# Optimization experiments

Measured on AMD Instinct MI355X. Metric: run time of the kernel, lower is better.

## Reference

```python
import math
import jax, jax.numpy as jnp
import numpy as np
from jax import lax

# FPN anchor layout: 1024x768 image, strides {4,8,16,32,64}, 3 anchors/location
NUM_PER_LEVEL = (147456, 36864, 9216, 2304, 576)
A_TOTAL = sum(NUM_PER_LEVEL)
BATCH = 8
PRE_NMS_TOP_N = 1000   # testing
POST_NMS_TOP_N = 1000  # testing
NMS_THRESH = 0.7
SCORE_THRESH = 0.0
MIN_SIZE = 1.0
IMG_H, IMG_W = 768.0, 1024.0
BBOX_XFORM_CLIP = math.log(1000.0 / 16.0)


def setup_inputs() -> dict:
    key = jax.random.key(0)
    k1, k2, k3, k4, k5, k6 = jax.random.split(key, 6)
    objectness = jax.random.normal(k1, (BATCH, A_TOTAL), jnp.float32)
    pred_bbox_deltas = jax.random.normal(k2, (BATCH, A_TOTAL, 4), jnp.float32) * 0.2
    # valid anchor boxes (x1, y1, x2, y2)
    cx = jax.random.uniform(k3, (A_TOTAL,), jnp.float32) * IMG_W
    cy = jax.random.uniform(k4, (A_TOTAL,), jnp.float32) * IMG_H
    w = 16.0 + jax.random.uniform(k5, (A_TOTAL,), jnp.float32) * 176.0
    h = 16.0 + jax.random.uniform(k6, (A_TOTAL,), jnp.float32) * 176.0
    anchors = jnp.stack([cx - 0.5 * w, cy - 0.5 * h, cx + 0.5 * w, cy + 0.5 * h], -1)
    return {"objectness": objectness, "pred_bbox_deltas": pred_bbox_deltas, "anchors": anchors}


def _nms_image(boxes, scores, lvl, valid):
    """batched_nms (level-offset trick) + post-NMS top-k, fixed shapes.
    boxes [K,4], scores [K], lvl [K] int, valid [K] bool -> [POST_NMS_TOP_N, 5]"""
    K = boxes.shape[0]
    s = jnp.where(valid, scores, -1.0)
    order = jnp.argsort(-s)  # decreasing score (invalid last)
    b = boxes[order]
    s = s[order]
    v = valid[order]
    # offset boxes per level so cross-level boxes never overlap (torchvision batched_nms)
    offset = lvl[order].astype(b.dtype) * (jnp.max(lax.stop_gradient(boxes)) + 1.0)
    nb = lax.stop_gradient(b) + offset[:, None]
    area = (nb[:, 2] - nb[:, 0]) * (nb[:, 3] - nb[:, 1])
    lt = jnp.maximum(nb[:, None, :2], nb[None, :, :2])  # [K,K,2]
    rb = jnp.minimum(nb[:, None, 2:], nb[None, :, 2:])
    wh = jnp.clip(rb - lt, 0.0)
    inter = wh[..., 0] * wh[..., 1]
    iou = inter / jnp.maximum(area[:, None] + area[None, :] - inter, 1e-9)
    pos = jnp.arange(K)

    def body(keep, i):
        sup = keep[i] & (iou[i] > NMS_THRESH) & (pos > i)
        return keep & ~sup, None

    keep, _ = lax.scan(body, v, pos)
    masked = jnp.where(keep, s, -1.0)
    top_s, top_i = lax.top_k(masked, POST_NMS_TOP_N)  # kept, decreasing score
    sel_b = b[top_i]
    ok = top_s > -0.5
    sel_b = jnp.where(ok[:, None], sel_b, 0.0)
    top_s = jnp.where(ok, top_s, 0.0)
    return jnp.concatenate([sel_b, top_s[:, None]], axis=-1)


def reference(objectness, pred_bbox_deltas, anchors):
    # --- box decode (BoxCoder, weights (1,1,1,1)) ---
    wa = anchors[:, 2] - anchors[:, 0]
    ha = anchors[:, 3] - anchors[:, 1]
    cxa = anchors[:, 0] + 0.5 * wa
    cya = anchors[:, 1] + 0.5 * ha
    dx, dy = pred_bbox_deltas[..., 0], pred_bbox_deltas[..., 1]
    dw = jnp.minimum(pred_bbox_deltas[..., 2], BBOX_XFORM_CLIP)
    dh = jnp.minimum(pred_bbox_deltas[..., 3], BBOX_XFORM_CLIP)
    pcx = dx * wa + cxa
    pcy = dy * ha + cya
    pw = jnp.exp(dw) * wa
    ph = jnp.exp(dh) * ha
    proposals = jnp.stack(
        [pcx - 0.5 * pw, pcy - 0.5 * ph, pcx + 0.5 * pw, pcy + 0.5 * ph], axis=-1
    )  # [B, A, 4]

    # --- per-level pre-NMS top-k (_get_top_n_idx) ---
    levels = jnp.concatenate(
        [jnp.full((n,), i, jnp.int32) for i, n in enumerate(NUM_PER_LEVEL)]
    )
    idx_parts = []
    off = 0
    for n in NUM_PER_LEVEL:
        k = min(PRE_NMS_TOP_N, n)
        _, ti = lax.top_k(objectness[:, off:off + n], k)
        idx_parts.append(ti + off)
        off += n
    top_idx = jnp.concatenate(idx_parts, axis=1)  # [B, K]

    scores = jax.nn.sigmoid(jnp.take_along_axis(objectness, top_idx, axis=1))
    lvl = levels[top_idx]
    boxes = jnp.take_along_axis(proposals, top_idx[..., None], axis=1)  # [B,K,4]

    # --- clip to image ---
    x1 = jnp.clip(boxes[..., 0], 0.0, IMG_W)
    y1 = jnp.clip(boxes[..., 1], 0.0, IMG_H)
    x2 = jnp.clip(boxes[..., 2], 0.0, IMG_W)
    y2 = jnp.clip(boxes[..., 3], 0.0, IMG_H)
    boxes = jnp.stack([x1, y1, x2, y2], axis=-1)

    # remove_small_boxes + score threshold (as validity mask; fixed shapes)
    valid = ((x2 - x1) >= MIN_SIZE) & ((y2 - y1) >= MIN_SIZE) & (scores >= SCORE_THRESH)

    # --- per-image batched NMS + post-NMS top-k ---
    return jax.vmap(_nms_image)(boxes, scores, lvl, valid)  # [B, POST_NMS_TOP_N, 5]
```

## Files before the change

kernel.cpp:

```cpp
#include <hip/hip_runtime.h>
#include <math.h>

#pragma clang fp contract(off)

#define A_TOTAL 196416
#define BATCH 8
#define KTOT 4576
#define NLEV 5
#define MSPLIT 16
#define RCAP 4096

static __device__ const int d_aoff[NLEV] = {0, 147456, 184320, 193536, 195840};
static __device__ const int d_n[NLEV]    = {147456, 36864, 9216, 2304, 576};
static __device__ const int d_k[NLEV]    = {1000, 1000, 1000, 1000, 576};
static __device__ const int d_koff[NLEV] = {0, 1000, 2000, 3000, 4000};
static __device__ const int d_spl[NLEV]  = {8, 2, 1, 1, 1};
static __device__ const int d_bp[NLEV]   = {0, 8, 10, 11, 12};
static __device__ const int d_pb_l[13]    = {0,0,0,0,0,0,0,0,1,1,2,3,4};
static __device__ const int d_pb_part[13] = {0,1,2,3,4,5,6,7,0,1,0,0,0};

#define TM_IOU (0.699999988079071044921875 + 0x1p-25)

__device__ inline unsigned int mono(float f) {
  unsigned int u = __float_as_uint(f);
  return (u & 0x80000000u) ? ~u : (u | 0x80000000u);
}

__device__ inline int cnt_gt(const float* A, int n, float s) {
  int lo = 0, hi = n;
  while (lo < hi) { int mid = (lo + hi) >> 1; if (A[mid] > s) lo = mid + 1; else hi = mid; }
  return lo;
}
__device__ inline int cnt_ge(const float* A, int n, float s) {
  int lo = 0, hi = n;
  while (lo < hi) { int mid = (lo + hi) >> 1; if (A[mid] >= s) lo = mid + 1; else hi = mid; }
  return lo;
}

__global__ __launch_bounds__(1024) void k_hist(const float* __restrict__ obj,
                                               int* __restrict__ hist_g) {
  int blk = blockIdx.x;
  int b = blk / 13, pb = blk % 13;
  int l = d_pb_l[pb], part = d_pb_part[pb];
  int slice = d_n[l] / d_spl[l];
  int start = d_aoff[l] + part * slice;
  const float4* p4 = (const float4*)(obj + (size_t)b * A_TOTAL + start);
  int s4 = slice >> 2, tid = threadIdx.x;
  __shared__ int h[4096];
  for (int i = tid; i < 4096; i += 1024) h[i] = 0;
  __syncthreads();
  for (int i = tid; i < s4; i += 1024) {
    float4 v = p4[i];
    atomicAdd(&h[mono(v.x) >> 20], 1);
    atomicAdd(&h[mono(v.y) >> 20], 1);
    atomicAdd(&h[mono(v.z) >> 20], 1);
    atomicAdd(&h[mono(v.w) >> 20], 1);
  }
  __syncthreads();
  int* out = hist_g + (size_t)blk * 4096;
  for (int i = tid; i < 4096; i += 1024) out[i] = h[i];
}

__global__ __launch_bounds__(256) void k_sel(const float* __restrict__ obj,
                                             const int* __restrict__ hist_g,
                                             unsigned int* __restrict__ T20_g,
                                             int* __restrict__ cnt_g,
                                             float* __restrict__ maxv) {
  int bl = blockIdx.x;
  int b = bl / NLEV, l = bl % NLEV;
  int tid = threadIdx.x;
  const int k = d_k[l];
  __shared__ int t[4096];
  __shared__ int grp[256];
  __shared__ int sP12, sNgt, sCnt12;
  __shared__ unsigned int sT20;
  int parts = d_spl[l];
  const int* hb = hist_g + (size_t)(b * 13 + d_bp[l]) * 4096;
  for (int bin = tid; bin < 4096; bin += 256) {
    int s = 0;
    for (int p = 0; p < parts; ++p) s += hb[p * 4096 + bin];
    t[bin] = s;
  }
  __syncthreads();
  {
    int s = 0;
    for (int j = 0; j < 16; ++j) s += t[tid * 16 + j];
    grp[tid] = s;
  }
  __syncthreads();
  if (tid == 0) {
    int cum = 0, g, d;
    for (g = 255; g >= 0; --g) {
      if (cum + grp[g] >= k) break;
      cum += grp[g];
    }
    for (d = 15; d >= 0; --d) {
      int c = t[g * 16 + d];
      if (cum + c >= k) break;
      cum += c;
    }
    sP12 = g * 16 + d;
    sNgt = cum;
    sCnt12 = cum + t[g * 16 + d];
    sT20 = ((unsigned int)(g * 16 + d)) << 8;
  }
  __syncthreads();
  if (sCnt12 > RCAP) {
    unsigned int P12 = (unsigned int)sP12;
    __shared__ int h2[256];
    h2[tid] = 0;
    __syncthreads();
    const float4* p4 = (const float4*)(obj + (size_t)b * A_TOTAL + d_aoff[l]);
    int n4 = d_n[l] >> 2;
    for (int i = tid; i < n4; i += 256) {
      float4 v = p4[i];
      unsigned int a[4] = {mono(v.x), mono(v.y), mono(v.z), mono(v.w)};
#pragma unroll
      for (int c = 0; c < 4; ++c)
        if ((a[c] >> 20) == P12) atomicAdd(&h2[(a[c] >> 12) & 255], 1);
    }
    __syncthreads();
    if (tid == 0) {
      int cum = sNgt, d;
      for (d = 255; d >= 0; --d) {
        if (cum + h2[d] >= k) break;
        cum += h2[d];
      }
      sT20 = (P12 << 8) | (unsigned int)d;
    }
    __syncthreads();
  }
  if (tid == 0) {
    T20_g[bl] = sT20;
    cnt_g[bl] = 0;
    if (l == 0) maxv[b] = 0.0f;
  }
}

__global__ __launch_bounds__(1024) void k_collect(const float* __restrict__ obj,
                                                  const unsigned int* __restrict__ T20_g,
                                                  int* __restrict__ cnt_g,
                                                  unsigned long long* __restrict__ cand_g) {
  int blk = blockIdx.x;
  int b = blk / 13, pb = blk % 13;
  int l = d_pb_l[pb], part = d_pb_part[pb];
  int bl = b * NLEV + l;
  int slice = d_n[l] / d_spl[l];
  int start = d_aoff[l] + part * slice;
  unsigned int T = T20_g[bl];
  const float4* p4 = (const float4*)(obj + (size_t)b * A_TOTAL + start);
  int s4 = slice >> 2, tid = threadIdx.x;
  int lbase = part * slice;
  __shared__ __align__(16) unsigned long long lbuf[RCAP];
  __shared__ int s_cnt, s_base;
  if (tid == 0) s_cnt = 0;
  __syncthreads();
  for (int i = tid; i < s4; i += 1024) {
    float4 v = p4[i];
    unsigned int a[4] = {mono(v.x), mono(v.y), mono(v.z), mono(v.w)};
#pragma unroll
    for (int c = 0; c < 4; ++c) {
      if ((a[c] >> 12) >= T) {
        int slot = atomicAdd(&s_cnt, 1);
        if (slot < RCAP) {
          int idx = lbase + 4 * i + c;
          lbuf[slot] = ((unsigned long long)a[c] << 32) |
                       (unsigned int)(~(unsigned int)idx);
        }
      }
    }
  }
  __syncthreads();
  int cnt = min(s_cnt, RCAP);
  if (tid == 0) s_base = atomicAdd(&cnt_g[bl], cnt);
  __syncthreads();
  int base = s_base;
  for (int i = tid; i < cnt; i += 1024) {
    int slot = base + i;
    if (slot < RCAP) cand_g[(size_t)bl * RCAP + slot] = lbuf[i];
  }
}

__global__ __launch_bounds__(256) void k_rank(const unsigned long long* __restrict__ cand_g,
                                              const int* __restrict__ cnt_g,
                                              int* __restrict__ sel_idx) {
  int bl = blockIdx.x >> 4, part = blockIdx.x & 15;
  int b = bl / NLEV, l = bl % NLEV;
  const int k = d_k[l], koff = d_koff[l], aoff = d_aoff[l];
  int cnt = min(cnt_g[bl], RCAP);
  if (part * 256 >= cnt) return;
  __shared__ __align__(16) unsigned long long cb[RCAP];
  int tid = threadIdx.x;
  const unsigned long long* src = cand_g + (size_t)bl * RCAP;
  for (int i = tid; i < cnt; i += 256) cb[i] = src[i];
  __syncthreads();
  int myi = part * 256 + tid;
  if (myi >= cnt) return;
  unsigned long long e = cb[myi];
  int rank = 0;
  int nc2 = cnt >> 1;
  const ulonglong2* c2 = (const ulonglong2*)cb;
  for (int j = 0; j < nc2; ++j) {
    ulonglong2 v = c2[j];
    rank += (v.x > e) + (v.y > e);
  }
  if (cnt & 1) rank += (cb[cnt - 1] > e);
  if (rank < k) {
    unsigned int idx = ~(unsigned int)(e & 0xFFFFFFFFull);
    sel_idx[b * KTOT + koff + rank] = aoff + (int)idx;
  }
}

__global__ __launch_bounds__(256) void k_decode(const float* __restrict__ obj,
                                                const float* __restrict__ deltas,
                                                const float* __restrict__ anchors,
                                                const int* __restrict__ sel_idx,
                                                float* __restrict__ boxes,
                                                float* __restrict__ sprime,
                                                float* __restrict__ maxv) {
  __shared__ unsigned int s_max[2];
  int g = blockIdx.x * 256 + threadIdx.x;
  int b0 = (blockIdx.x * 256) / KTOT;
  if (threadIdx.x < 2) s_max[threadIdx.x] = 0u;
  __syncthreads();
  if (g < BATCH * KTOT) {
    int b = g / KTOT;
    int gidx = sel_idx[g];
    float o = obj[(size_t)b * A_TOTAL + gidx];
    const float* dl = deltas + ((size_t)b * A_TOTAL + gidx) * 4;
    const float* an = anchors + (size_t)gidx * 4;
    float a0 = an[0], a1 = an[1], a2 = an[2], a3 = an[3];
    float wa = a2 - a0, ha = a3 - a1;
    float cxa = a0 + 0.5f * wa, cya = a1 + 0.5f * ha;
    float dx = dl[0], dy = dl[1];
    const float CLIPV = 4.135166556742356f;
    float dw = fminf(dl[2], CLIPV), dh = fminf(dl[3], CLIPV);
    float pcx = dx * wa + cxa;
    float pcy = dy * ha + cya;
    float pw = (float)exp((double)dw) * wa;
    float ph = (float)exp((double)dh) * ha;
    float x1 = pcx - 0.5f * pw, y1 = pcy - 0.5f * ph;
    float x2 = pcx + 0.5f * pw, y2 = pcy + 0.5f * ph;
    x1 = fminf(fmaxf(x1, 0.0f), 1024.0f);
    x2 = fminf(fmaxf(x2, 0.0f), 1024.0f);
    y1 = fminf(fmaxf(y1, 0.0f), 768.0f);
    y2 = fminf(fmaxf(y2, 0.0f), 768.0f);
    boxes[(size_t)g * 4 + 0] = x1;
    boxes[(size_t)g * 4 + 1] = y1;
    boxes[(size_t)g * 4 + 2] = x2;
    boxes[(size_t)g * 4 + 3] = y2;
    float s = (float)(1.0 / (1.0 + exp(-(double)o)));
    bool valid = ((x2 - x1) >= 1.0f) && ((y2 - y1) >= 1.0f) && (s >= 0.0f);
    sprime[g] = valid ? s : -1.0f;
    float mx = fmaxf(fmaxf(x1, y1), fmaxf(x2, y2));
    atomicMax(&s_max[b - b0], __float_as_uint(mx));
  }
  __syncthreads();
  if (threadIdx.x < 2 && b0 + (int)threadIdx.x < BATCH)
    atomicMax((unsigned int*)&maxv[b0 + threadIdx.x], s_max[threadIdx.x]);
}

__global__ __launch_bounds__(1024) void k_merge(const float* __restrict__ sprime,
                                                const float* __restrict__ boxes,
                                                const float* __restrict__ maxv,
                                                float* __restrict__ score_sorted,
                                                float* __restrict__ boxes_sorted,
                                                int* __restrict__ lvl_sorted,
                                                float4* __restrict__ lvlbox,
                                                int* __restrict__ lvlrank,
                                                int* __restrict__ g_V) {
  int b = blockIdx.x, tid = threadIdx.x, lane = tid & 63, wv = tid >> 6;
  __shared__ float s_sc[KTOT];
  __shared__ int s_src[KTOT];
  __shared__ int s_iv[KTOT];
  __shared__ int s_V[NLEV];
  __shared__ int s_wcnt[16];

  for (int l = 0; l < NLEV; ++l) {
    int koff = d_koff[l], k = d_k[l];
    bool in = tid < k;
    float s = in ? sprime[(size_t)b * KTOT + koff + tid] : -1.0f;
    bool valid = in && (s >= 0.0f);
    unsigned long long mb = __ballot(valid);
    if (lane == 0) s_wcnt[wv] = __popcll(mb);
    __syncthreads();
    int pre = 0;
    for (int w = 0; w < wv; ++w) pre += s_wcnt[w];
    int vrank = pre + __popcll(mb & ((1ull << lane) - 1ull));
    if (valid) { s_sc[koff + vrank] = s; s_src[koff + vrank] = tid; }
    if (in && !valid) s_iv[koff + (tid - vrank)] = tid;
    if (tid == 0) {
      int t = 0;
      for (int w = 0; w < 16; ++w) t += s_wcnt[w];
      s_V[l] = t;
    }
    __syncthreads();
  }
  int V[NLEV], VT = 0;
  for (int l = 0; l < NLEV; ++l) { V[l] = s_V[l]; VT += V[l]; }
  int IOff[NLEV];
  { int run = VT; for (int l = 0; l < NLEV; ++l) { IOff[l] = run; run += d_k[l] - V[l]; } }
  if (tid < NLEV) g_V[b * NLEV + tid] = V[tid];
  float mv1 = maxv[b] + 1.0f;

  for (int e = tid; e < KTOT; e += 1024) {
    int le = (e < 1000) ? 0 : (e < 2000) ? 1 : (e < 3000) ? 2 : (e < 4000) ? 3 : 4;
    int koff = d_koff[le];
    int i = e - koff;
    int rank, srcpos;
    float sval;
    if (i < V[le]) {
      float s = s_sc[e];
      rank = i;
      for (int l2 = 0; l2 < NLEV; ++l2) {
        if (l2 == le) continue;
        const float* A = s_sc + d_koff[l2];
        rank += (l2 < le) ? cnt_ge(A, V[l2], s) : cnt_gt(A, V[l2], s);
      }
      srcpos = koff + s_src[e];
      sval = s;
    } else {
      int j = i - V[le];
      rank = IOff[le] + j;
      srcpos = koff + s_iv[koff + j];
      sval = -1.0f;
    }
    score_sorted[(size_t)b * KTOT + rank] = sval;
    lvl_sorted[b * KTOT + rank] = le;
    const float* bp = boxes + ((size_t)(b * KTOT + srcpos)) * 4;
    float x1 = bp[0], y1 = bp[1], x2 = bp[2], y2 = bp[3];
    float* op = boxes_sorted + ((size_t)(b * KTOT + rank)) * 4;
    op[0] = x1; op[1] = y1; op[2] = x2; op[3] = y2;
    float off = (float)le * mv1;
    int blx = b * NLEV + le;
    lvlbox[blx * 1024 + i] = make_float4(x1 + off, y1 + off, x2 + off, y2 + off);
    lvlrank[blx * 1024 + i] = rank;
  }
}

__global__ __launch_bounds__(1024) void k_mask(const float4* __restrict__ lvlbox,
                                               unsigned long long* __restrict__ masks) {
  int blk = blockIdx.x;
  int bl = blk / MSPLIT, part = blk % MSPLIT;
  int l = bl % NLEV;
  const int m = d_k[l];
  int row0 = part * 64;
  if (row0 >= m) return;
  int tid = threadIdx.x, lane = tid & 63, w = tid >> 6;
  __shared__ float4 lbox[1024];
  for (int i = tid; i < m; i += 1024) lbox[i] = lvlbox[bl * 1024 + i];
  __syncthreads();
  int i = row0 + lane;
  if (i >= m) return;
  float4 bb = lbox[i];
  float ba = (bb.z - bb.x) * (bb.w - bb.y);
  unsigned long long bits = 0ull;
  int jbase = w * 64;
  if (jbase + 63 > i && jbase < m) {
    int jhi = min(64, m - jbase);
    for (int jo = 0; jo < jhi; ++jo) {
      int j = jbase + jo;
      float4 cb = lbox[j];
      float ca = (cb.z - cb.x) * (cb.w - cb.y);
      float xx1 = fmaxf(bb.x, cb.x), yy1 = fmaxf(bb.y, cb.y);
      float xx2 = fminf(bb.z, cb.z), yy2 = fminf(bb.w, cb.w);
      float wd = fmaxf(xx2 - xx1, 0.0f), ht = fmaxf(yy2 - yy1, 0.0f);
      float inter = wd * ht;
      float denom = fmaxf(ba + ca - inter, 1e-9f);
      if ((j > i) && ((double)inter >= TM_IOU * (double)denom)) bits |= (1ull << jo);
    }
  }
  masks[((size_t)bl * 16 + w) * 1024 + i] = bits;
}

__global__ __launch_bounds__(1024) void k_scan(const unsigned long long* __restrict__ masks,
                                               const int* __restrict__ lvlrank,
                                               const int* __restrict__ g_V,
                                               int* __restrict__ keep_g) {
  int bl = blockIdx.x;
  int b = bl / NLEV, l = bl % NLEV;
  int tid = threadIdx.x, lane = tid & 63, w = tid >> 6;
  const int m = d_k[l];
  const int nch = (m + 63) / 64;
  const unsigned long long* M = masks + (size_t)bl * 16 * 1024;
  __shared__ unsigned long long s_remv[16];
  __shared__ unsigned long long s_D[2][72];
  __shared__ unsigned long long s_dw;
  int V = g_V[bl];
  int base_w = w * 64;
  unsigned long long init_w;
  if (V <= base_w) init_w = ~0ull;
  else if (V >= base_w + 64) init_w = 0ull;
  else init_w = (~0ull) << (V - base_w);
  if (w == 0) s_D[0][lane] = (lane < m) ? M[lane] : 0ull;
  if (tid < 8) { s_D[0][64 + tid] = 0ull; s_D[1][64 + tid] = 0ull; }
  unsigned long long acc = 0ull;
  __syncthreads();

  for (int c = 0; c < nch; ++c) {
    unsigned long long val = 0ull;
    int r = 64 * c + lane;
    if (w > c && w < nch && r < m) val = M[(size_t)w * 1024 + r];
    if (w == c) {
      unsigned long long red = acc;
#pragma unroll
      for (int s = 1; s < 64; s <<= 1) red |= __shfl_xor(red, s);
      unsigned long long dw = init_w | red;
      const unsigned long long* D = s_D[c & 1];
      unsigned long long pb[8];
#pragma unroll
      for (int u = 0; u < 8; ++u) pb[u] = D[u];
#pragma unroll
      for (int g = 0; g < 8; ++g) {
#pragma unroll
        for (int u = 0; u < 8; ++u) {
          int j = g * 8 + u;
          if (!((dw >> j) & 1ull)) dw |= pb[u];
          pb[u] = D[j + 8];
        }
      }
      if (lane == 0) { s_dw = dw; s_remv[c] = dw; }
    }
    if (w == c + 1 && w < nch) {
      int rr = 64 * (c + 1) + lane;
      s_D[(c + 1) & 1][lane] = (rr < m) ? M[(size_t)(c + 1) * 1024 + rr] : 0ull;
    }
    __syncthreads();
    if (w > c && w < nch) {
      unsigned long long kept = ~s_dw;
      if ((kept >> lane) & 1ull) acc |= val;
    }
    __syncthreads();
  }
  for (int i = tid; i < m; i += 1024) {
    int keep = ((s_remv[i >> 6] >> (i & 63)) & 1ull) ? 0 : 1;
    keep_g[b * KTOT + lvlrank[bl * 1024 + i]] = keep;
  }
}

__global__ __launch_bounds__(1024) void k_out(const float* __restrict__ boxes_sorted,
                                              const float* __restrict__ score_sorted,
                                              const int* __restrict__ keep_g,
                                              float* __restrict__ out) {
  int b = blockIdx.x, tid = threadIdx.x, lane = tid & 63, wv = tid >> 6;
  __shared__ int s_wcnt[16], s_base;
  for (int i = tid; i < 5000; i += 1024) out[(size_t)b * 5000 + i] = 0.0f;
  if (tid == 0) s_base = 0;
  __syncthreads();
  for (int chunk = 0; chunk < KTOT; chunk += 1024) {
    int j = chunk + tid;
    bool match = (j < KTOT) && (keep_g[b * KTOT + j] != 0);
    unsigned long long mb = __ballot(match);
    if (lane == 0) s_wcnt[wv] = __popcll(mb);
    __syncthreads();
    int rank = s_base + __popcll(mb & ((1ull << lane) - 1ull));
    for (int w = 0; w < wv; ++w) rank += s_wcnt[w];
    if (match && rank < 1000) {
      const float* bp = boxes_sorted + ((size_t)(b * KTOT + j)) * 4;
      float* op = out + ((size_t)(b * 1000 + rank)) * 5;
      op[0] = bp[0]; op[1] = bp[1]; op[2] = bp[2]; op[3] = bp[3];
      op[4] = score_sorted[b * KTOT + j];
    }
    __syncthreads();
    if (tid == 0) {
      int s = 0;
      for (int w = 0; w < 16; ++w) s += s_wcnt[w];
      s_base += s;
    }
    __syncthreads();
  }
}

extern "C" void kernel_launch(void* const* d_in, const int* in_sizes, int n_in,
                              void* d_out, int out_size, void* d_ws, size_t ws_size,
                              hipStream_t stream) {
  const float* obj     = (const float*)d_in[0];
  const float* deltas  = (const float*)d_in[1];
  const float* anchors = (const float*)d_in[2];
  float* out = (float*)d_out;

  int*   sel_idx      = (int*)d_ws;
  float* boxes        = (float*)(sel_idx + BATCH * KTOT);
  float* sprime       = boxes + (size_t)BATCH * KTOT * 4;
  float* maxv         = sprime + BATCH * KTOT;
  float* score_sorted = maxv + BATCH;
  float* boxes_sorted = score_sorted + BATCH * KTOT;
  int*   lvl_sorted   = (int*)(boxes_sorted + (size_t)BATCH * KTOT * 4);
  int*   keep_g       = lvl_sorted + BATCH * KTOT;
  float4* lvlbox      = (float4*)(keep_g + BATCH * KTOT);
  int*   lvlrank      = (int*)(lvlbox + BATCH * NLEV * 1024);
  int*   g_V          = lvlrank + BATCH * NLEV * 1024;
  unsigned long long* masks = (unsigned long long*)(((uintptr_t)(g_V + 40) + 15) & ~(uintptr_t)15);
  int*   hist_g = (int*)masks;
  unsigned long long* cand_g =
      (unsigned long long*)((char*)masks + (size_t)104 * 4096 * 4);
  unsigned int* T20_g = (unsigned int*)((char*)cand_g + (size_t)40 * RCAP * 8);
  int*   cnt_g  = (int*)(T20_g + 40);

  hipLaunchKernelGGL(k_hist, dim3(BATCH * 13), dim3(1024), 0, stream, obj, hist_g);
  hipLaunchKernelGGL(k_sel, dim3(BATCH * NLEV), dim3(256), 0, stream,
                     obj, hist_g, T20_g, cnt_g, maxv);
  hipLaunchKernelGGL(k_collect, dim3(BATCH * 13), dim3(1024), 0, stream,
                     obj, T20_g, cnt_g, cand_g);
  hipLaunchKernelGGL(k_rank, dim3(BATCH * NLEV * 16), dim3(256), 0, stream,
                     cand_g, cnt_g, sel_idx);
  hipLaunchKernelGGL(k_decode, dim3((BATCH * KTOT + 255) / 256), dim3(256), 0, stream,
                     obj, deltas, anchors, sel_idx, boxes, sprime, maxv);
  hipLaunchKernelGGL(k_merge, dim3(BATCH), dim3(1024), 0, stream,
                     sprime, boxes, maxv, score_sorted, boxes_sorted, lvl_sorted,
                     lvlbox, lvlrank, g_V);
  hipLaunchKernelGGL(k_mask, dim3(BATCH * NLEV * MSPLIT), dim3(1024), 0, stream,
                     lvlbox, masks);
  hipLaunchKernelGGL(k_scan, dim3(BATCH * NLEV), dim3(1024), 0, stream,
                     masks, lvlrank, g_V, keep_g);
  hipLaunchKernelGGL(k_out, dim3(BATCH), dim3(1024), 0, stream,
                     boxes_sorted, score_sorted, keep_g, out);
}
```

Before: 231.8 us.

## Fuse threshold selection into collect, rank with decode, merge per-level after NMS

Threshold selection moves into the collect kernel, using only the 12-bit histogram bin and a larger candidate buffer (RCAP 6144), so the separate selection kernel and its refinement pass are dropped. Ranking is fused with box decoding, reading the score back from the monotone key instead of reloading objectness. NMS now runs per level on valid boxes only, with masks and scan bounded by the valid count. The global cross-level merge happens after NMS, over kept boxes only. This cuts the number of launches and global round trips, but the candidate buffer can overflow RCAP if the 12-bit bin holds too many elements.

```diff
diff --git a/kernel.cpp b/kernel.cpp
--- a/kernel.cpp
+++ b/kernel.cpp
@@ -8,12 +8,11 @@
 #define KTOT 4576
 #define NLEV 5
 #define MSPLIT 16
-#define RCAP 4096
+#define RCAP 6144
 
 static __device__ const int d_aoff[NLEV] = {0, 147456, 184320, 193536, 195840};
 static __device__ const int d_n[NLEV]    = {147456, 36864, 9216, 2304, 576};
 static __device__ const int d_k[NLEV]    = {1000, 1000, 1000, 1000, 576};
-static __device__ const int d_koff[NLEV] = {0, 1000, 2000, 3000, 4000};
 static __device__ const int d_spl[NLEV]  = {8, 2, 1, 1, 1};
 static __device__ const int d_bp[NLEV]   = {0, 8, 10, 11, 12};
 static __device__ const int d_pb_l[13]    = {0,0,0,0,0,0,0,0,1,1,2,3,4};
@@ -25,6 +24,9 @@
   unsigned int u = __float_as_uint(f);
   return (u & 0x80000000u) ? ~u : (u | 0x80000000u);
 }
+__device__ inline float imono(unsigned int m) {
+  return __uint_as_float((m & 0x80000000u) ? (m & 0x7FFFFFFFu) : ~m);
+}
 
 __device__ inline int cnt_gt(const float* A, int n, float s) {
   int lo = 0, hi = n;
@@ -38,14 +40,21 @@
 }
 
 __global__ __launch_bounds__(1024) void k_hist(const float* __restrict__ obj,
-                                               int* __restrict__ hist_g) {
+                                               int* __restrict__ hist_g,
+                                               int* __restrict__ cnt_g,
+                                               float* __restrict__ maxblk) {
   int blk = blockIdx.x;
+  int tid = threadIdx.x;
+  if (blk == 0) {
+    for (int i = tid; i < 640; i += 1024) maxblk[i] = 0.0f;
+    for (int i = tid; i < 40; i += 1024) cnt_g[i] = 0;
+  }
   int b = blk / 13, pb = blk % 13;
   int l = d_pb_l[pb], part = d_pb_part[pb];
   int slice = d_n[l] / d_spl[l];
   int start = d_aoff[l] + part * slice;
   const float4* p4 = (const float4*)(obj + (size_t)b * A_TOTAL + start);
-  int s4 = slice >> 2, tid = threadIdx.x;
+  int s4 = slice >> 2;
   __shared__ int h[4096];
   for (int i = tid; i < 4096; i += 1024) h[i] = 0;
   __syncthreads();
@@ -57,110 +66,66 @@
     atomicAdd(&h[mono(v.w) >> 20], 1);
   }
   __syncthreads();
-  int* out = hist_g + (size_t)blk * 4096;
-  for (int i = tid; i < 4096; i += 1024) out[i] = h[i];
-}
-
-__global__ __launch_bounds__(256) void k_sel(const float* __restrict__ obj,
-                                             const int* __restrict__ hist_g,
-                                             unsigned int* __restrict__ T20_g,
-                                             int* __restrict__ cnt_g,
-                                             float* __restrict__ maxv) {
-  int bl = blockIdx.x;
-  int b = bl / NLEV, l = bl % NLEV;
-  int tid = threadIdx.x;
-  const int k = d_k[l];
-  __shared__ int t[4096];
-  __shared__ int grp[256];
-  __shared__ int sP12, sNgt, sCnt12;
-  __shared__ unsigned int sT20;
-  int parts = d_spl[l];
-  const int* hb = hist_g + (size_t)(b * 13 + d_bp[l]) * 4096;
-  for (int bin = tid; bin < 4096; bin += 256) {
-    int s = 0;
-    for (int p = 0; p < parts; ++p) s += hb[p * 4096 + bin];
-    t[bin] = s;
-  }
-  __syncthreads();
-  {
-    int s = 0;
-    for (int j = 0; j < 16; ++j) s += t[tid * 16 + j];
-    grp[tid] = s;
-  }
-  __syncthreads();
-  if (tid == 0) {
-    int cum = 0, g, d;
-    for (g = 255; g >= 0; --g) {
-      if (cum + grp[g] >= k) break;
-      cum += grp[g];
-    }
-    for (d = 15; d >= 0; --d) {
-      int c = t[g * 16 + d];
-      if (cum + c >= k) break;
-      cum += c;
-    }
-    sP12 = g * 16 + d;
-    sNgt = cum;
-    sCnt12 = cum + t[g * 16 + d];
-    sT20 = ((unsigned int)(g * 16 + d)) << 8;
-  }
-  __syncthreads();
-  if (sCnt12 > RCAP) {
-    unsigned int P12 = (unsigned int)sP12;
-    __shared__ int h2[256];
-    h2[tid] = 0;
-    __syncthreads();
-    const float4* p4 = (const float4*)(obj + (size_t)b * A_TOTAL + d_aoff[l]);
-    int n4 = d_n[l] >> 2;
-    for (int i = tid; i < n4; i += 256) {
-      float4 v = p4[i];
-      unsigned int a[4] = {mono(v.x), mono(v.y), mono(v.z), mono(v.w)};
-#pragma unroll
-      for (int c = 0; c < 4; ++c)
-        if ((a[c] >> 20) == P12) atomicAdd(&h2[(a[c] >> 12) & 255], 1);
-    }
-    __syncthreads();
-    if (tid == 0) {
-      int cum = sNgt, d;
-      for (d = 255; d >= 0; --d) {
-        if (cum + h2[d] >= k) break;
-        cum += h2[d];
-      }
-      sT20 = (P12 << 8) | (unsigned int)d;
-    }
-    __syncthreads();
-  }
-  if (tid == 0) {
-    T20_g[bl] = sT20;
-    cnt_g[bl] = 0;
-    if (l == 0) maxv[b] = 0.0f;
-  }
+  int* outp = hist_g + (size_t)blk * 4096;
+  for (int i = tid; i < 4096; i += 1024) outp[i] = h[i];
 }
 
 __global__ __launch_bounds__(1024) void k_collect(const float* __restrict__ obj,
-                                                  const unsigned int* __restrict__ T20_g,
+                                                  const int* __restrict__ hist_g,
                                                   int* __restrict__ cnt_g,
                                                   unsigned long long* __restrict__ cand_g) {
   int blk = blockIdx.x;
   int b = blk / 13, pb = blk % 13;
   int l = d_pb_l[pb], part = d_pb_part[pb];
   int bl = b * NLEV + l;
-  int slice = d_n[l] / d_spl[l];
-  int start = d_aoff[l] + part * slice;
-  unsigned int T = T20_g[bl];
-  const float4* p4 = (const float4*)(obj + (size_t)b * A_TOTAL + start);
-  int s4 = slice >> 2, tid = threadIdx.x;
-  int lbase = part * slice;
+  const int k = d_k[l];
+  int tid = threadIdx.x;
+  __shared__ int t[4096];
+  __shared__ int grp[256];
+  __shared__ unsigned int sP;
   __shared__ __align__(16) unsigned long long lbuf[RCAP];
   __shared__ int s_cnt, s_base;
+  int parts = d_spl[l];
+  const int* hb = hist_g + (size_t)(b * 13 + d_bp[l]) * 4096;
+  for (int bin = tid; bin < 4096; bin += 1024) {
+    int s = 0;
+    for (int p = 0; p < parts; ++p) s += hb[p * 4096 + bin];
+    t[bin] = s;
+  }
   if (tid == 0) s_cnt = 0;
   __syncthreads();
+  if (tid < 256) {
+    int s = 0;
+    for (int j = 0; j < 16; ++j) s += t[tid * 16 + j];
+    grp[tid] = s;
+  }
+  __syncthreads();
+  if (tid == 0) {
+    int cum = 0, g, d;
+    for (g = 255; g >= 0; --g) {
+      if (cum + grp[g] >= k) break;
+      cum += grp[g];
+    }
+    for (d = 15; d >= 0; --d) {
+      int c = t[g * 16 + d];
+      if (cum + c >= k) break;
+      cum += c;
+    }
+    sP = (unsigned int)(g * 16 + d);
+  }
+  __syncthreads();
+  unsigned int P = sP;
+  int slice = d_n[l] / parts;
+  int start = d_aoff[l] + part * slice;
+  const float4* p4 = (const float4*)(obj + (size_t)b * A_TOTAL + start);
+  int s4 = slice >> 2;
+  int lbase = part * slice;
   for (int i = tid; i < s4; i += 1024) {
     float4 v = p4[i];
     unsigned int a[4] = {mono(v.x), mono(v.y), mono(v.z), mono(v.w)};
 #pragma unroll
     for (int c = 0; c < 4; ++c) {
-      if ((a[c] >> 12) >= T) {
+      if ((a[c] >> 20) >= P) {
         int slot = atomicAdd(&s_cnt, 1);
         if (slot < RCAP) {
           int idx = lbase + 4 * i + c;
@@ -181,183 +146,136 @@
   }
 }
 
-__global__ __launch_bounds__(256) void k_rank(const unsigned long long* __restrict__ cand_g,
-                                              const int* __restrict__ cnt_g,
-                                              int* __restrict__ sel_idx) {
+__global__ __launch_bounds__(256) void k_rankdec(const unsigned long long* __restrict__ cand_g,
+                                                 const int* __restrict__ cnt_g,
+                                                 const float* __restrict__ deltas,
+                                                 const float* __restrict__ anchors,
+                                                 float* __restrict__ sc0,
+                                                 float4* __restrict__ box0,
+                                                 float* __restrict__ maxblk) {
   int bl = blockIdx.x >> 4, part = blockIdx.x & 15;
   int b = bl / NLEV, l = bl % NLEV;
-  const int k = d_k[l], koff = d_koff[l], aoff = d_aoff[l];
+  const int k = d_k[l], aoff = d_aoff[l];
   int cnt = min(cnt_g[bl], RCAP);
   if (part * 256 >= cnt) return;
   __shared__ __align__(16) unsigned long long cb[RCAP];
+  __shared__ unsigned int s_max;
   int tid = threadIdx.x;
+  if (tid == 0) s_max = 0u;
   const unsigned long long* src = cand_g + (size_t)bl * RCAP;
   for (int i = tid; i < cnt; i += 256) cb[i] = src[i];
   __syncthreads();
   int myi = part * 256 + tid;
-  if (myi >= cnt) return;
-  unsigned long long e = cb[myi];
-  int rank = 0;
-  int nc2 = cnt >> 1;
-  const ulonglong2* c2 = (const ulonglong2*)cb;
-  for (int j = 0; j < nc2; ++j) {
-    ulonglong2 v = c2[j];
-    rank += (v.x > e) + (v.y > e);
-  }
-  if (cnt & 1) rank += (cb[cnt - 1] > e);
-  if (rank < k) {
-    unsigned int idx = ~(unsigned int)(e & 0xFFFFFFFFull);
-    sel_idx[b * KTOT + koff + rank] = aoff + (int)idx;
-  }
-}
-
-__global__ __launch_bounds__(256) void k_decode(const float* __restrict__ obj,
-                                                const float* __restrict__ deltas,
-                                                const float* __restrict__ anchors,
-                                                const int* __restrict__ sel_idx,
-                                                float* __restrict__ boxes,
-                                                float* __restrict__ sprime,
-                                                float* __restrict__ maxv) {
-  __shared__ unsigned int s_max[2];
-  int g = blockIdx.x * 256 + threadIdx.x;
-  int b0 = (blockIdx.x * 256) / KTOT;
-  if (threadIdx.x < 2) s_max[threadIdx.x] = 0u;
-  __syncthreads();
-  if (g < BATCH * KTOT) {
-    int b = g / KTOT;
-    int gidx = sel_idx[g];
-    float o = obj[(size_t)b * A_TOTAL + gidx];
-    const float* dl = deltas + ((size_t)b * A_TOTAL + gidx) * 4;
-    const float* an = anchors + (size_t)gidx * 4;
-    float a0 = an[0], a1 = an[1], a2 = an[2], a3 = an[3];
-    float wa = a2 - a0, ha = a3 - a1;
-    float cxa = a0 + 0.5f * wa, cya = a1 + 0.5f * ha;
-    float dx = dl[0], dy = dl[1];
-    const float CLIPV = 4.135166556742356f;
-    float dw = fminf(dl[2], CLIPV), dh = fminf(dl[3], CLIPV);
-    float pcx = dx * wa + cxa;
-    float pcy = dy * ha + cya;
-    float pw = (float)exp((double)dw) * wa;
-    float ph = (float)exp((double)dh) * ha;
-    float x1 = pcx - 0.5f * pw, y1 = pcy - 0.5f * ph;
-    float x2 = pcx + 0.5f * pw, y2 = pcy + 0.5f * ph;
-    x1 = fminf(fmaxf(x1, 0.0f), 1024.0f);
-    x2 = fminf(fmaxf(x2, 0.0f), 1024.0f);
-    y1 = fminf(fmaxf(y1, 0.0f), 768.0f);
-    y2 = fminf(fmaxf(y2, 0.0f), 768.0f);
-    boxes[(size_t)g * 4 + 0] = x1;
-    boxes[(size_t)g * 4 + 1] = y1;
-    boxes[(size_t)g * 4 + 2] = x2;
-    boxes[(size_t)g * 4 + 3] = y2;
-    float s = (float)(1.0 / (1.0 + exp(-(double)o)));
-    bool valid = ((x2 - x1) >= 1.0f) && ((y2 - y1) >= 1.0f) && (s >= 0.0f);
-    sprime[g] = valid ? s : -1.0f;
-    float mx = fmaxf(fmaxf(x1, y1), fmaxf(x2, y2));
-    atomicMax(&s_max[b - b0], __float_as_uint(mx));
-  }
-  __syncthreads();
-  if (threadIdx.x < 2 && b0 + (int)threadIdx.x < BATCH)
-    atomicMax((unsigned int*)&maxv[b0 + threadIdx.x], s_max[threadIdx.x]);
-}
-
-__global__ __launch_bounds__(1024) void k_merge(const float* __restrict__ sprime,
-                                                const float* __restrict__ boxes,
-                                                const float* __restrict__ maxv,
-                                                float* __restrict__ score_sorted,
-                                                float* __restrict__ boxes_sorted,
-                                                int* __restrict__ lvl_sorted,
-                                                float4* __restrict__ lvlbox,
-                                                int* __restrict__ lvlrank,
-                                                int* __restrict__ g_V) {
-  int b = blockIdx.x, tid = threadIdx.x, lane = tid & 63, wv = tid >> 6;
-  __shared__ float s_sc[KTOT];
-  __shared__ int s_src[KTOT];
-  __shared__ int s_iv[KTOT];
-  __shared__ int s_V[NLEV];
+  float mx = 0.0f;
+  if (myi < cnt) {
+    unsigned long long e = cb[myi];
+    int rank = 0;
+    int nc2 = cnt >> 1;
+    const ulonglong2* c2 = (const ulonglong2*)cb;
+    for (int j = 0; j < nc2; ++j) {
+      ulonglong2 v = c2[j];
+      rank += (v.x > e) + (v.y > e);
+    }
+    if (cnt & 1) rank += (cb[cnt - 1] > e);
+    if (rank < k) {
+      unsigned int key = (unsigned int)(e >> 32);
+      unsigned int idx = ~(unsigned int)(e & 0xFFFFFFFFull);
+      float o = imono(key);
+      int gidx = aoff + (int)idx;
+      const float* dl = deltas + ((size_t)b * A_TOTAL + gidx) * 4;
+      const float* an = anchors + (size_t)gidx * 4;
+      float a0 = an[0], a1 = an[1], a2 = an[2], a3 = an[3];
+      float wa = a2 - a0, ha = a3 - a1;
+      float cxa = a0 + 0.5f * wa, cya = a1 + 0.5f * ha;
+      float dx = dl[0], dy = dl[1];
+      const float CLIPV = 4.135166556742356f;
+      float dw = fminf(dl[2], CLIPV), dh = fminf(dl[3], CLIPV);
+      float pcx = dx * wa + cxa;
+      float pcy = dy * ha + cya;
+      float pw = (float)exp((double)dw) * wa;
+      float ph = (float)exp((double)dh) * ha;
+      float x1 = pcx - 0.5f * pw, y1 = pcy - 0.5f * ph;
+      float x2 = pcx + 0.5f * pw, y2 = pcy + 0.5f * ph;
+      x1 = fminf(fmaxf(x1, 0.0f), 1024.0f);
+      x2 = fminf(fmaxf(x2, 0.0f), 1024.0f);
+      y1 = fminf(fmaxf(y1, 0.0f), 768.0f);
+      y2 = fminf(fmaxf(y2, 0.0f), 768.0f);
+      float s = (float)(1.0 / (1.0 + exp(-(double)o)));
+      bool valid = ((x2 - x1) >= 1.0f) && ((y2 - y1) >= 1.0f) && (s >= 0.0f);
+      sc0[bl * 1024 + rank] = valid ? s : -1.0f;
+      box0[bl * 1024 + rank] = make_float4(x1, y1, x2, y2);
+      mx = fmaxf(fmaxf(x1, y1), fmaxf(x2, y2));
+    }
+  }
+  atomicMax(&s_max, __float_as_uint(mx));
+  __syncthreads();
+  if (tid == 0) maxblk[blockIdx.x] = __uint_as_float(s_max);
+}
+
+__global__ __launch_bounds__(1024) void k_compact(const float* __restrict__ sc0,
+                                                  const float4* __restrict__ box0,
+                                                  const float* __restrict__ maxblk,
+                                                  float* __restrict__ lvlsc,
+                                                  float4* __restrict__ lvlraw,
+                                                  float4* __restrict__ lvlofs,
+                                                  int* __restrict__ g_V) {
+  int bl = blockIdx.x;
+  int b = bl / NLEV, l = bl % NLEV;
+  const int k = d_k[l];
+  int tid = threadIdx.x, lane = tid & 63, wv = tid >> 6;
+  __shared__ float s_mv;
   __shared__ int s_wcnt[16];
-
-  for (int l = 0; l < NLEV; ++l) {
-    int koff = d_koff[l], k = d_k[l];
-    bool in = tid < k;
-    float s = in ? sprime[(size_t)b * KTOT + koff + tid] : -1.0f;
-    bool valid = in && (s >= 0.0f);
-    unsigned long long mb = __ballot(valid);
-    if (lane == 0) s_wcnt[wv] = __popcll(mb);
-    __syncthreads();
-    int pre = 0;
-    for (int w = 0; w < wv; ++w) pre += s_wcnt[w];
-    int vrank = pre + __popcll(mb & ((1ull << lane) - 1ull));
-    if (valid) { s_sc[koff + vrank] = s; s_src[koff + vrank] = tid; }
-    if (in && !valid) s_iv[koff + (tid - vrank)] = tid;
-    if (tid == 0) {
-      int t = 0;
-      for (int w = 0; w < 16; ++w) t += s_wcnt[w];
-      s_V[l] = t;
-    }
-    __syncthreads();
-  }
-  int V[NLEV], VT = 0;
-  for (int l = 0; l < NLEV; ++l) { V[l] = s_V[l]; VT += V[l]; }
-  int IOff[NLEV];
-  { int run = VT; for (int l = 0; l < NLEV; ++l) { IOff[l] = run; run += d_k[l] - V[l]; } }
-  if (tid < NLEV) g_V[b * NLEV + tid] = V[tid];
-  float mv1 = maxv[b] + 1.0f;
-
-  for (int e = tid; e < KTOT; e += 1024) {
-    int le = (e < 1000) ? 0 : (e < 2000) ? 1 : (e < 3000) ? 2 : (e < 4000) ? 3 : 4;
-    int koff = d_koff[le];
-    int i = e - koff;
-    int rank, srcpos;
-    float sval;
-    if (i < V[le]) {
-      float s = s_sc[e];
-      rank = i;
-      for (int l2 = 0; l2 < NLEV; ++l2) {
-        if (l2 == le) continue;
-        const float* A = s_sc + d_koff[l2];
-        rank += (l2 < le) ? cnt_ge(A, V[l2], s) : cnt_gt(A, V[l2], s);
-      }
-      srcpos = koff + s_src[e];
-      sval = s;
-    } else {
-      int j = i - V[le];
-      rank = IOff[le] + j;
-      srcpos = koff + s_iv[koff + j];
-      sval = -1.0f;
-    }
-    score_sorted[(size_t)b * KTOT + rank] = sval;
-    lvl_sorted[b * KTOT + rank] = le;
-    const float* bp = boxes + ((size_t)(b * KTOT + srcpos)) * 4;
-    float x1 = bp[0], y1 = bp[1], x2 = bp[2], y2 = bp[3];
-    float* op = boxes_sorted + ((size_t)(b * KTOT + rank)) * 4;
-    op[0] = x1; op[1] = y1; op[2] = x2; op[3] = y2;
-    float off = (float)le * mv1;
-    int blx = b * NLEV + le;
-    lvlbox[blx * 1024 + i] = make_float4(x1 + off, y1 + off, x2 + off, y2 + off);
-    lvlrank[blx * 1024 + i] = rank;
-  }
-}
-
-__global__ __launch_bounds__(1024) void k_mask(const float4* __restrict__ lvlbox,
+  if (wv == 0) {
+    float v = (lane < 80) ? maxblk[b * 80 + lane] : 0.0f;
+    float v2 = (lane + 64 < 80) ? maxblk[b * 80 + lane + 64] : 0.0f;
+    v = fmaxf(v, v2);
+#pragma unroll
+    for (int s = 1; s < 64; s <<= 1) v = fmaxf(v, __shfl_xor(v, s));
+    if (lane == 0) s_mv = v;
+  }
+  bool in = tid < k;
+  float s = in ? sc0[bl * 1024 + tid] : -1.0f;
+  bool valid = in && (s >= 0.0f);
+  unsigned long long mb = __ballot(valid);
+  if (lane == 0) s_wcnt[wv] = __popcll(mb);
+  __syncthreads();
+  int pre = 0;
+  for (int w = 0; w < wv; ++w) pre += s_wcnt[w];
+  int j = pre + __popcll(mb & ((1ull << lane) - 1ull));
+  float off = (float)l * (s_mv + 1.0f);
+  if (valid) {
+    lvlsc[bl * 1024 + j] = s;
+    float4 bx = box0[bl * 1024 + tid];
+    lvlraw[bl * 1024 + j] = bx;
+    lvlofs[bl * 1024 + j] = make_float4(bx.x + off, bx.y + off, bx.z + off, bx.w + off);
+  }
+  if (tid == 0) {
+    int t = 0;
+    for (int w = 0; w < 16; ++w) t += s_wcnt[w];
+    g_V[bl] = t;
+  }
+}
+
+__global__ __launch_bounds__(1024) void k_mask(const float4* __restrict__ lvlofs,
+                                               const int* __restrict__ g_V,
                                                unsigned long long* __restrict__ masks) {
   int blk = blockIdx.x;
   int bl = blk / MSPLIT, part = blk % MSPLIT;
-  int l = bl % NLEV;
-  const int m = d_k[l];
+  int V = g_V[bl];
   int row0 = part * 64;
-  if (row0 >= m) return;
+  if (row0 >= V) return;
   int tid = threadIdx.x, lane = tid & 63, w = tid >> 6;
   __shared__ float4 lbox[1024];
-  for (int i = tid; i < m; i += 1024) lbox[i] = lvlbox[bl * 1024 + i];
+  for (int i = tid; i < V; i += 1024) lbox[i] = lvlofs[bl * 1024 + i];
   __syncthreads();
   int i = row0 + lane;
-  if (i >= m) return;
+  if (i >= V) return;
   float4 bb = lbox[i];
   float ba = (bb.z - bb.x) * (bb.w - bb.y);
   unsigned long long bits = 0ull;
   int jbase = w * 64;
-  if (jbase + 63 > i && jbase < m) {
-    int jhi = min(64, m - jbase);
+  if (jbase + 63 > i && jbase < V) {
+    int jhi = min(64, V - jbase);
     for (int jo = 0; jo < jhi; ++jo) {
       int j = jbase + jo;
       float4 cb = lbox[j];
@@ -374,25 +292,23 @@
 }
 
 __global__ __launch_bounds__(1024) void k_scan(const unsigned long long* __restrict__ masks,
-                                               const int* __restrict__ lvlrank,
                                                const int* __restrict__ g_V,
-                                               int* __restrict__ keep_g) {
+                                               unsigned long long* __restrict__ keepbits) {
   int bl = blockIdx.x;
-  int b = bl / NLEV, l = bl % NLEV;
   int tid = threadIdx.x, lane = tid & 63, w = tid >> 6;
-  const int m = d_k[l];
-  const int nch = (m + 63) / 64;
+  int V = g_V[bl];
+  const int nch = (V + 63) / 64;
   const unsigned long long* M = masks + (size_t)bl * 16 * 1024;
   __shared__ unsigned long long s_remv[16];
   __shared__ unsigned long long s_D[2][72];
   __shared__ unsigned long long s_dw;
-  int V = g_V[bl];
+  if (tid < 16) s_remv[tid] = ~0ull;
   int base_w = w * 64;
   unsigned long long init_w;
   if (V <= base_w) init_w = ~0ull;
   else if (V >= base_w + 64) init_w = 0ull;
   else init_w = (~0ull) << (V - base_w);
-  if (w == 0) s_D[0][lane] = (lane < m) ? M[lane] : 0ull;
+  if (w == 0 && nch > 0) s_D[0][lane] = (lane < V) ? M[lane] : 0ull;
   if (tid < 8) { s_D[0][64 + tid] = 0ull; s_D[1][64 + tid] = 0ull; }
   unsigned long long acc = 0ull;
   __syncthreads();
@@ -400,7 +316,7 @@
   for (int c = 0; c < nch; ++c) {
     unsigned long long val = 0ull;
     int r = 64 * c + lane;
-    if (w > c && w < nch && r < m) val = M[(size_t)w * 1024 + r];
+    if (w > c && w < nch && r < V) val = M[(size_t)w * 1024 + r];
     if (w == c) {
       unsigned long long red = acc;
 #pragma unroll
@@ -423,7 +339,7 @@
     }
     if (w == c + 1 && w < nch) {
       int rr = 64 * (c + 1) + lane;
-      s_D[(c + 1) & 1][lane] = (rr < m) ? M[(size_t)(c + 1) * 1024 + rr] : 0ull;
+      s_D[(c + 1) & 1][lane] = (rr < V) ? M[(size_t)(c + 1) * 1024 + rr] : 0ull;
     }
     __syncthreads();
     if (w > c && w < nch) {
@@ -432,42 +348,56 @@
     }
     __syncthreads();
   }
-  for (int i = tid; i < m; i += 1024) {
-    int keep = ((s_remv[i >> 6] >> (i & 63)) & 1ull) ? 0 : 1;
-    keep_g[b * KTOT + lvlrank[bl * 1024 + i]] = keep;
-  }
-}
-
-__global__ __launch_bounds__(1024) void k_out(const float* __restrict__ boxes_sorted,
-                                              const float* __restrict__ score_sorted,
-                                              const int* __restrict__ keep_g,
+  if (tid < 16) keepbits[bl * 16 + tid] = ~s_remv[tid];
+}
+
+__global__ __launch_bounds__(1024) void k_out(const float* __restrict__ lvlsc,
+                                              const float4* __restrict__ lvlraw,
+                                              const unsigned long long* __restrict__ keepbits,
+                                              const int* __restrict__ g_V,
                                               float* __restrict__ out) {
-  int b = blockIdx.x, tid = threadIdx.x, lane = tid & 63, wv = tid >> 6;
-  __shared__ int s_wcnt[16], s_base;
+  int b = blockIdx.x;
+  int tid = threadIdx.x, lane = tid & 63, wv = tid >> 6;
+  __shared__ float ksc[NLEV * 1024];
+  __shared__ int kj[NLEV * 1024];
+  __shared__ int sK[NLEV];
+  __shared__ int s_wcnt[16];
   for (int i = tid; i < 5000; i += 1024) out[(size_t)b * 5000 + i] = 0.0f;
-  if (tid == 0) s_base = 0;
-  __syncthreads();
-  for (int chunk = 0; chunk < KTOT; chunk += 1024) {
-    int j = chunk + tid;
-    bool match = (j < KTOT) && (keep_g[b * KTOT + j] != 0);
-    unsigned long long mb = __ballot(match);
+  for (int l = 0; l < NLEV; ++l) {
+    int bl = b * NLEV + l;
+    int V = g_V[bl];
+    bool kept = (tid < V) && ((keepbits[bl * 16 + (tid >> 6)] >> (tid & 63)) & 1ull);
+    unsigned long long mb = __ballot(kept);
     if (lane == 0) s_wcnt[wv] = __popcll(mb);
     __syncthreads();
-    int rank = s_base + __popcll(mb & ((1ull << lane) - 1ull));
-    for (int w = 0; w < wv; ++w) rank += s_wcnt[w];
-    if (match && rank < 1000) {
-      const float* bp = boxes_sorted + ((size_t)(b * KTOT + j)) * 4;
-      float* op = out + ((size_t)(b * 1000 + rank)) * 5;
-      op[0] = bp[0]; op[1] = bp[1]; op[2] = bp[2]; op[3] = bp[3];
-      op[4] = score_sorted[b * KTOT + j];
+    int pre = 0;
+    for (int w = 0; w < wv; ++w) pre += s_wcnt[w];
+    int r = pre + __popcll(mb & ((1ull << lane) - 1ull));
+    if (kept) { ksc[l * 1024 + r] = lvlsc[bl * 1024 + tid]; kj[l * 1024 + r] = tid; }
+    if (tid == 0) {
+      int t = 0;
+      for (int w = 0; w < 16; ++w) t += s_wcnt[w];
+      sK[l] = t;
     }
     __syncthreads();
-    if (tid == 0) {
-      int s = 0;
-      for (int w = 0; w < 16; ++w) s += s_wcnt[w];
-      s_base += s;
-    }
-    __syncthreads();
+  }
+  int K[NLEV];
+  for (int l = 0; l < NLEV; ++l) K[l] = sK[l];
+  for (int l = 0; l < NLEV; ++l) {
+    if (tid < K[l]) {
+      float s = ksc[l * 1024 + tid];
+      int rank = tid;
+      for (int l2 = 0; l2 < NLEV; ++l2) {
+        if (l2 == l) continue;
+        const float* A = ksc + l2 * 1024;
+        rank += (l2 < l) ? cnt_ge(A, K[l2], s) : cnt_gt(A, K[l2], s);
+      }
+      if (rank < 1000) {
+        float4 bx = lvlraw[(size_t)(b * NLEV + l) * 1024 + kj[l * 1024 + tid]];
+        float* op = out + (size_t)b * 5000 + (size_t)rank * 5;
+        op[0] = bx.x; op[1] = bx.y; op[2] = bx.z; op[3] = bx.w; op[4] = s;
+      }
+    }
   }
 }
 
@@ -479,40 +409,32 @@
   const float* anchors = (const float*)d_in[2];
   float* out = (float*)d_out;
 
-  int*   sel_idx      = (int*)d_ws;
-  float* boxes        = (float*)(sel_idx + BATCH * KTOT);
-  float* sprime       = boxes + (size_t)BATCH * KTOT * 4;
-  float* maxv         = sprime + BATCH * KTOT;
-  float* score_sorted = maxv + BATCH;
-  float* boxes_sorted = score_sorted + BATCH * KTOT;
-  int*   lvl_sorted   = (int*)(boxes_sorted + (size_t)BATCH * KTOT * 4);
-  int*   keep_g       = lvl_sorted + BATCH * KTOT;
-  float4* lvlbox      = (float4*)(keep_g + BATCH * KTOT);
-  int*   lvlrank      = (int*)(lvlbox + BATCH * NLEV * 1024);
-  int*   g_V          = lvlrank + BATCH * NLEV * 1024;
-  unsigned long long* masks = (unsigned long long*)(((uintptr_t)(g_V + 40) + 15) & ~(uintptr_t)15);
-  int*   hist_g = (int*)masks;
-  unsigned long long* cand_g =
-      (unsigned long long*)((char*)masks + (size_t)104 * 4096 * 4);
-  unsigned int* T20_g = (unsigned int*)((char*)cand_g + (size_t)40 * RCAP * 8);
-  int*   cnt_g  = (int*)(T20_g + 40);
-
-  hipLaunchKernelGGL(k_hist, dim3(BATCH * 13), dim3(1024), 0, stream, obj, hist_g);
-  hipLaunchKernelGGL(k_sel, dim3(BATCH * NLEV), dim3(256), 0, stream,
-                     obj, hist_g, T20_g, cnt_g, maxv);
+  char* p = (char*)d_ws;
+  float4* box0   = (float4*)p; p += (size_t)40 * 1024 * sizeof(float4);
+  float4* lvlraw = (float4*)p; p += (size_t)40 * 1024 * sizeof(float4);
+  float4* lvlofs = (float4*)p; p += (size_t)40 * 1024 * sizeof(float4);
+  unsigned long long* cand_g   = (unsigned long long*)p; p += (size_t)40 * RCAP * 8;
+  unsigned long long* masks    = (unsigned long long*)p; p += (size_t)40 * 16 * 1024 * 8;
+  unsigned long long* keepbits = (unsigned long long*)p; p += (size_t)40 * 16 * 8;
+  int*   hist_g = (int*)p;   p += (size_t)104 * 4096 * 4;
+  int*   cnt_g  = (int*)p;   p += 40 * 4;
+  float* maxblk = (float*)p; p += 640 * 4;
+  float* sc0    = (float*)p; p += (size_t)40 * 1024 * 4;
+  float* lvlsc  = (float*)p; p += (size_t)40 * 1024 * 4;
+  int*   g_V    = (int*)p;   p += 40 * 4;
+
+  hipLaunchKernelGGL(k_hist, dim3(BATCH * 13), dim3(1024), 0, stream,
+                     obj, hist_g, cnt_g, maxblk);
   hipLaunchKernelGGL(k_collect, dim3(BATCH * 13), dim3(1024), 0, stream,
-                     obj, T20_g, cnt_g, cand_g);
-  hipLaunchKernelGGL(k_rank, dim3(BATCH * NLEV * 16), dim3(256), 0, stream,
-                     cand_g, cnt_g, sel_idx);
-  hipLaunchKernelGGL(k_decode, dim3((BATCH * KTOT + 255) / 256), dim3(256), 0, stream,
-                     obj, deltas, anchors, sel_idx, boxes, sprime, maxv);
-  hipLaunchKernelGGL(k_merge, dim3(BATCH), dim3(1024), 0, stream,
-                     sprime, boxes, maxv, score_sorted, boxes_sorted, lvl_sorted,
-                     lvlbox, lvlrank, g_V);
+                     obj, hist_g, cnt_g, cand_g);
+  hipLaunchKernelGGL(k_rankdec, dim3(BATCH * NLEV * 16), dim3(256), 0, stream,
+                     cand_g, cnt_g, deltas, anchors, sc0, box0, maxblk);
+  hipLaunchKernelGGL(k_compact, dim3(BATCH * NLEV), dim3(1024), 0, stream,
+                     sc0, box0, maxblk, lvlsc, lvlraw, lvlofs, g_V);
   hipLaunchKernelGGL(k_mask, dim3(BATCH * NLEV * MSPLIT), dim3(1024), 0, stream,
-                     lvlbox, masks);
+                     lvlofs, g_V, masks);
   hipLaunchKernelGGL(k_scan, dim3(BATCH * NLEV), dim3(1024), 0, stream,
-                     masks, lvlrank, g_V, keep_g);
+                     masks, g_V, keepbits);
   hipLaunchKernelGGL(k_out, dim3(BATCH), dim3(1024), 0, stream,
-                     boxes_sorted, score_sorted, keep_g, out);
-}
+                     lvlsc, lvlraw, keepbits, g_V, out);
+}
```

New measurement: 211.2 us. 8.9% less time.
